# Kernel tuning notes

Measured on AMD Instinct MI355X. Metric: run time of the kernel, lower is better.

The kernel has to match this reference:

```python
import jax, jax.numpy as jnp
import numpy as np

COLOR_SIZE = 8
FILTERS = 64
LAYERS = 4
CUMSUM_NORM = 256 * 256 * 3  # hardcoded in original: /256/256/3


def setup_inputs() -> dict:
    key = jax.random.key(0)
    k0, k1, k2, k3 = jax.random.split(key, 4)
    s = 0.05
    example = jax.random.randint(k0, (4, 256, 256, 3), 0, COLOR_SIZE, dtype=jnp.int32)
    # per-channel Dense stacks: layer 0 has input dim 1, layers 1..3 have input dim FILTERS
    W_in_first = jax.random.normal(k1, (3, 1, FILTERS), dtype=jnp.float32) * s
    b_in_first = jnp.zeros((3, FILTERS), dtype=jnp.float32)
    W_in_rest = jax.random.normal(k2, (LAYERS - 1, 3, FILTERS, FILTERS), dtype=jnp.float32) * s
    b_in_rest = jnp.zeros((LAYERS - 1, 3, FILTERS), dtype=jnp.float32)
    W_final = jax.random.normal(k3, (3, FILTERS, COLOR_SIZE), dtype=jnp.float32) * s
    b_final = jnp.zeros((3, COLOR_SIZE), dtype=jnp.float32)
    return {
        "example": example,
        "W_in_first": W_in_first, "b_in_first": b_in_first,
        "W_in_rest": W_in_rest, "b_in_rest": b_in_rest,
        "W_final": W_final, "b_final": b_final,
    }


def reference(example, W_in_first, b_in_first, W_in_rest, b_in_rest, W_final, b_final):
    # example: [B, H, W, 3] int in [0, COLOR_SIZE)
    x = example.astype(jnp.float32) / COLOR_SIZE * 2.0 - 1.0
    B, H, W, _ = x.shape
    L = H * W
    x = x.reshape(B, L, 3, 1)

    def layer(x, Wl, bl):
        # per-channel dense + relu: [B, L, 3, din] x [3, din, dout] -> [B, L, 3, dout]
        x = jax.nn.relu(jnp.einsum('blcd,cde->blce', x, Wl) + bl)
        # flatten channels into the sequence and take causal running sum
        x = x.reshape(B, L * 3, FILTERS)
        x = jnp.cumsum(x, axis=-2) / CUMSUM_NORM
        return x.reshape(B, L, 3, FILTERS)

    x = layer(x, W_in_first, b_in_first)
    for i in range(LAYERS - 1):
        x = layer(x, W_in_rest[i], b_in_rest[i])

    # final per-channel dense to color logits (no activation)
    x = jnp.einsum('blcd,cde->blce', x, W_final) + b_final
    return x.reshape(B, H, W, 3, COLOR_SIZE)
```

## Files before the change

### kernel.cpp

```cpp
#include <hip/hip_runtime.h>
#include <stdint.h>


#define BB   4
#define SP   65536
#define SS   196608
#define CC   1024
#define NBLK (BB * CC)
#define INVN (1.0f / 196608.0f)

typedef __attribute__((ext_vector_type(8))) _Float16 half8;
typedef __attribute__((ext_vector_type(4))) float    f32x4;

__global__ __launch_bounds__(256)
void prep(const float* __restrict__ W0, const float* __restrict__ b0,
          const float* __restrict__ Wr, const float* __restrict__ Wfin,
          float* __restrict__ Wt32, _Float16* __restrict__ Wt16,
          float* __restrict__ Wf, float* __restrict__ tab)
{
    int i = blockIdx.x * 256 + threadIdx.x;
    int nth = gridDim.x * 256;
    for (int idx = i; idx < 36864; idx += nth) {
        int d = idx & 63, f = (idx >> 6) & 63, lc = idx >> 12;
        float v = Wr[(size_t)(lc * 64 + d) * 64 + f];
        Wt32[idx] = v;
        Wt16[idx] = (_Float16)v;
    }
    for (int idx = i; idx < 1536; idx += nth) {
        int d = idx & 63, k = (idx >> 6) & 7, c = idx >> 9;
        Wf[idx] = Wfin[(size_t)(c * 64 + d) * 8 + k];
    }
    for (int idx = i; idx < 1536; idx += nth) {
        int f = idx & 63, v = (idx >> 6) & 7, c = idx >> 9;
        float xv = v * 0.25f - 1.0f;
        tab[idx] = fmaxf(W0[c * 64 + f] * xv + b0[c * 64 + f], 0.f);
    }
}

__global__ __launch_bounds__(256)
void l0_kernel(const int* __restrict__ ex, _Float16* __restrict__ Y,
               float* __restrict__ A, const float* __restrict__ tab)
{
    __shared__ float stab[1536];
    __shared__ float seg[3][4][64];
    int tid = threadIdx.x;
    for (int i = tid; i < 1536; i += 256) stab[i] = tab[i];
    __syncthreads();

    int b = blockIdx.x / CC, ci = blockIdx.x % CC;
    int f = tid & 63, g = tid >> 6;
    int pixbase = ci * 64 + g * 16;

    float y[3][16];
#pragma unroll
    for (int p = 0; p < 16; ++p) {
        const int* ep = ex + ((size_t)b * SP + pixbase + p) * 3;
#pragma unroll
        for (int c = 0; c < 3; ++c) y[c][p] = stab[(c * 8 + ep[c]) * 64 + f];
    }
#pragma unroll
    for (int c = 0; c < 3; ++c)
#pragma unroll
        for (int p = 1; p < 16; ++p) y[c][p] += y[c][p - 1];

#pragma unroll
    for (int c = 0; c < 3; ++c) seg[c][g][f] = y[c][15];
    __syncthreads();

    float off[3];
#pragma unroll
    for (int c = 0; c < 3; ++c) {
        float o = 0.f;
        for (int g2 = 0; g2 < g; ++g2) o += seg[c][g2][f];
        off[c] = o;
    }
    if (g == 0) {
        float agg = 0.f;
#pragma unroll
        for (int c = 0; c < 3; ++c)
#pragma unroll
            for (int g2 = 0; g2 < 4; ++g2) agg += seg[c][g2][f];
        A[((size_t)b * CC + ci) * 64 + f] = agg;
    }

#pragma unroll
    for (int p = 0; p < 16; ++p) {
        float S0 = y[0][p] + off[0], S1 = y[1][p] + off[1], S2 = y[2][p] + off[2];
        float P1 = p ? y[1][p - 1] + off[1] : off[1];
        float P2 = p ? y[2][p - 1] + off[2] : off[2];
        float r0 = S0 + P1 + P2, r1 = S0 + S1 + P2, r2 = S0 + S1 + S2;
        size_t pix = (size_t)pixbase + p;
        Y[((size_t)(b * 3 + 0) * SP + pix) * 64 + f] = (_Float16)r0;
        Y[((size_t)(b * 3 + 1) * SP + pix) * 64 + f] = (_Float16)r1;
        Y[((size_t)(b * 3 + 2) * SP + pix) * 64 + f] = (_Float16)r2;
    }
}

__global__ __launch_bounds__(1024)
void scanA(const float* __restrict__ A, float* __restrict__ carry)
{
    __shared__ float seg[16][65];
    int b = blockIdx.x, tid = threadIdx.x;
    int f = tid & 63, g = tid >> 6;
    const float* ap = A + (size_t)b * CC * 64;
    float* cp = carry + (size_t)b * CC * 64;
    int j0 = g * 64;
    float sum = 0.f;
#pragma unroll 8
    for (int j = 0; j < 64; ++j) sum += ap[(size_t)(j0 + j) * 64 + f];
    seg[g][f] = sum;
    __syncthreads();
    float run = 0.f;
    for (int g2 = 0; g2 < g; ++g2) run += seg[g2][f];
    for (int j = 0; j < 64; ++j) {
        float v = ap[(size_t)(j0 + j) * 64 + f];
        cp[(size_t)(j0 + j) * 64 + f] = run;
        run += v;
    }
}

__global__ __launch_bounds__(256, 4)
void mid_mfma(const _Float16* Yin, _Float16* Yout,
              const float* __restrict__ carry, float* __restrict__ A,
              const _Float16* __restrict__ W16,
              const float* __restrict__ W32,
              const float* __restrict__ bias)
{
    __shared__ float seg[3][1040];
    __shared__ float basearr[3][64];
    __shared__ float tot[3][64];
    __shared__ _Float16 bounce[64 * 72];

    int b = blockIdx.x / CC, ci = blockIdx.x % CC;
    int tid = threadIdx.x;
    int w = tid >> 6, l = tid & 63;
    int lm = l & 15, lq = l >> 4;
    int p0 = ci * 64 + w * 16;

    if (tid < 192) {
        int c = tid >> 6, f = tid & 63;
        const float* cr = carry + ((size_t)b * CC + ci) * 64;
        const float* wp = W32 + (size_t)(c * 64 + f) * 64;
        float s0 = 0.f, s1 = 0.f, s2 = 0.f, s3 = 0.f;
#pragma unroll
        for (int d4 = 0; d4 < 16; ++d4) {
            float4 cv = *(const float4*)(cr + d4 * 4);
            float4 wv = *(const float4*)(wp + d4 * 4);
            s0 += cv.x * wv.x; s1 += cv.y * wv.y;
            s2 += cv.z * wv.z; s3 += cv.w * wv.w;
        }
        basearr[c][f] = bias[c * 64 + f] + INVN * ((s0 + s1) + (s2 + s3));
    }

    f32x4 acc[3][4];
#pragma unroll
    for (int c = 0; c < 3; ++c) {
        const _Float16* Yc = Yin + ((size_t)(b * 3 + c) * SP) * 64;
        const half8* ap = (const half8*)(Yc + (size_t)(p0 + lm) * 64);
        half8 a0 = ap[lq], a1 = ap[4 + lq];
#pragma unroll
        for (int nt = 0; nt < 4; ++nt) {
            const half8* bp = (const half8*)(W16 + (size_t)(c * 64 + nt * 16 + lm) * 64);
            half8 b0 = bp[lq], b1 = bp[4 + lq];
            f32x4 t = {0.f, 0.f, 0.f, 0.f};
            t = __builtin_amdgcn_mfma_f32_16x16x32_f16(a0, b0, t, 0, 0, 0);
            t = __builtin_amdgcn_mfma_f32_16x16x32_f16(a1, b1, t, 0, 0, 0);
            acc[c][nt] = t;
        }
    }
    __syncthreads();

    float s[3][4][4];
#pragma unroll
    for (int c = 0; c < 3; ++c) {
#pragma unroll
        for (int nt = 0; nt < 4; ++nt) {
            float base = basearr[c][nt * 16 + lm];
            float run = 0.f;
#pragma unroll
            for (int r = 0; r < 4; ++r) {
                float yv = fmaxf(base + INVN * acc[c][nt][r], 0.f);
                run += yv;
                s[c][nt][r] = run;
            }
            seg[c][(w * 4 + lq) * 65 + nt * 16 + lm] = run;
        }
    }
    __syncthreads();

    if (tid < 192) {
        int c = tid >> 6, f = tid & 63;
        float run = 0.f;
#pragma unroll
        for (int sg = 0; sg < 16; ++sg) {
            float v = seg[c][sg * 65 + f];
            seg[c][sg * 65 + f] = run;
            run += v;
        }
        tot[c][f] = run;
    }
    __syncthreads();
    if (tid < 64)
        A[((size_t)b * CC + ci) * 64 + tid] = tot[0][tid] + tot[1][tid] + tot[2][tid];

    float off[3][4];
#pragma unroll
    for (int c = 0; c < 3; ++c)
#pragma unroll
        for (int nt = 0; nt < 4; ++nt)
            off[c][nt] = seg[c][(w * 4 + lq) * 65 + nt * 16 + lm];

#pragma unroll
    for (int cs = 0; cs < 3; ++cs) {
#pragma unroll
        for (int nt = 0; nt < 4; ++nt) {
#pragma unroll
            for (int r = 0; r < 4; ++r) {
                float S0 = off[0][nt] + s[0][nt][r];
                float S1 = off[1][nt] + s[1][nt][r];
                float S2 = off[2][nt] + s[2][nt][r];
                float P1 = off[1][nt] + (r ? s[1][nt][r - 1] : 0.f);
                float P2 = off[2][nt] + (r ? s[2][nt][r - 1] : 0.f);
                float val = (cs == 0) ? S0 + P1 + P2
                          : (cs == 1) ? S0 + S1 + P2
                                      : S0 + S1 + S2;
                bounce[(w * 16 + lq * 4 + r) * 72 + nt * 16 + lm] = (_Float16)val;
            }
        }
        __syncthreads();
        _Float16* Yo = Yout + ((size_t)(b * 3 + cs) * SP + (size_t)ci * 64) * 64;
#pragma unroll
        for (int it = 0; it < 2; ++it) {
            int i8 = it * 256 + tid;
            int pix = i8 >> 3, f8 = i8 & 7;
            *((half8*)Yo + pix * 8 + f8) = *(const half8*)&bounce[pix * 72 + f8 * 8];
        }
        __syncthreads();
    }
}

__global__ __launch_bounds__(192)
void final_kernel(const _Float16* __restrict__ Yin,
                  const float* __restrict__ carry,
                  const float* __restrict__ Wf,
                  const float* __restrict__ bf,
                  float* __restrict__ out)
{
    __shared__ __align__(16) float swf[1536];
    __shared__ float scarry[64];
    __shared__ float pcd[24][8];
    __shared__ float scd[24];
    __shared__ float sbf[24];
    int b = blockIdx.x / CC, ci = blockIdx.x % CC;
    int tid = threadIdx.x;

    for (int i = tid; i < 1536; i += 192) swf[i] = Wf[i];
    if (tid < 64) scarry[tid] = carry[((size_t)b * CC + ci) * 64 + tid];
    if (tid < 24) sbf[tid] = bf[tid];
    __syncthreads();

    {
        int pair = tid >> 3, dg = tid & 7;
        float sx = 0.f;
#pragma unroll
        for (int dd = 0; dd < 8; ++dd) {
            int d = dg * 8 + dd;
            sx += scarry[d] * swf[pair * 64 + d];
        }
        pcd[pair][dg] = sx;
    }
    __syncthreads();
    if (tid < 24) {
        float t = 0.f;
#pragma unroll
        for (int j = 0; j < 8; ++j) t += pcd[tid][j];
        scd[tid] = t;
    }
    __syncthreads();

    int c = tid >> 6, j = tid & 63;
    const half8* xp = (const half8*)(Yin + ((size_t)(b * 3 + c) * SP + ci * 64 + j) * 64);
    half8 h[8];
#pragma unroll
    for (int i = 0; i < 8; ++i) h[i] = xp[i];
    float sk[8];
#pragma unroll
    for (int k = 0; k < 8; ++k) sk[k] = 0.f;
#pragma unroll
    for (int d4 = 0; d4 < 16; ++d4) {
        half8 hv = h[d4 >> 1];
        int o = (d4 & 1) * 4;
        float x0 = (float)hv[o], x1 = (float)hv[o + 1];
        float x2 = (float)hv[o + 2], x3 = (float)hv[o + 3];
#pragma unroll
        for (int k = 0; k < 8; ++k) {
            float4 wv = *(const float4*)&swf[(c * 8 + k) * 64 + d4 * 4];
            sk[k] += x0 * wv.x + x1 * wv.y + x2 * wv.z + x3 * wv.w;
        }
    }
    size_t pos = (size_t)b * SS + (size_t)(ci * 64 + j) * 3 + c;
    float* op = out + pos * 8;
    float o0[8];
#pragma unroll
    for (int k = 0; k < 8; ++k)
        o0[k] = sbf[c * 8 + k] + INVN * (scd[c * 8 + k] + sk[k]);
    *(float4*)(op + 0) = make_float4(o0[0], o0[1], o0[2], o0[3]);
    *(float4*)(op + 4) = make_float4(o0[4], o0[5], o0[6], o0[7]);
}

extern "C" void kernel_launch(void* const* d_in, const int* in_sizes, int n_in,
                              void* d_out, int out_size, void* d_ws, size_t ws_size,
                              hipStream_t stream)
{
    const int*   ex   = (const int*)d_in[0];
    const float* W0   = (const float*)d_in[1];
    const float* b0   = (const float*)d_in[2];
    const float* Wr   = (const float*)d_in[3];
    const float* br   = (const float*)d_in[4];
    const float* Wfin = (const float*)d_in[5];
    const float* bfin = (const float*)d_in[6];
    float* out = (float*)d_out;

    char* ws = (char*)d_ws;
    _Float16* Y = (_Float16*)ws;
    size_t off = (size_t)BB * 3 * SP * 64 * sizeof(_Float16);
    float* A     = (float*)(ws + off);  off += (size_t)BB * CC * 64 * 4;
    float* carry = (float*)(ws + off);  off += (size_t)BB * CC * 64 * 4;
    float* Wt32  = (float*)(ws + off);  off += 36864 * 4;
    float* Wf    = (float*)(ws + off);  off += 1536 * 4;
    float* tab   = (float*)(ws + off);  off += 1536 * 4;
    _Float16* Wt16 = (_Float16*)(ws + off); off += 36864 * 2;

    prep<<<64, 256, 0, stream>>>(W0, b0, Wr, Wfin, Wt32, Wt16, Wf, tab);
    l0_kernel<<<NBLK, 256, 0, stream>>>(ex, Y, A, tab);
    scanA<<<BB, 1024, 0, stream>>>(A, carry);
    for (int l = 0; l < 3; ++l) {
        mid_mfma<<<NBLK, 256, 0, stream>>>(Y, Y, carry, A,
                                           Wt16 + (size_t)l * 12288,
                                           Wt32 + (size_t)l * 12288,
                                           br + (size_t)l * 192);
        scanA<<<BB, 1024, 0, stream>>>(A, carry);
    }
    final_kernel<<<NBLK, 192, 0, stream>>>(Y, carry, Wf, bfin, out);
}
```

Baseline: 414.6 us.

## Process four chunks per block in mid layer with shuffle-based intra-block scan

The mid-layer kernel now handles four 64-pixel chunks per block, cutting the grid by four. Per-thread weight rows are loaded once into registers and reused for the four carry dot products. The LDS-based segment scan is replaced by wave shuffles plus a small per-wave totals table, and all three channel outputs are staged in one larger bounce buffer so they are written with fewer barriers. scanA also gets explicit batched loads for more memory-level parallelism. In exchange the kernel has fewer blocks to spread across the GPU, uses more LDS and registers, and runs its four chunks one after another inside each block.

```diff
diff --git a/kernel.cpp b/kernel.cpp
--- a/kernel.cpp
+++ b/kernel.cpp
@@ -6,7 +6,6 @@
 #define SP   65536
 #define SS   196608
 #define CC   1024
-#define NBLK (BB * CC)
 #define INVN (1.0f / 196608.0f)
 
 typedef __attribute__((ext_vector_type(8))) _Float16 half8;
@@ -106,114 +105,140 @@
     float* cp = carry + (size_t)b * CC * 64;
     int j0 = g * 64;
     float sum = 0.f;
-#pragma unroll 8
-    for (int j = 0; j < 64; ++j) sum += ap[(size_t)(j0 + j) * 64 + f];
+#pragma unroll
+    for (int j8 = 0; j8 < 8; ++j8) {
+        float v[8];
+#pragma unroll
+        for (int k = 0; k < 8; ++k) v[k] = ap[(size_t)(j0 + j8 * 8 + k) * 64 + f];
+#pragma unroll
+        for (int k = 0; k < 8; ++k) sum += v[k];
+    }
     seg[g][f] = sum;
     __syncthreads();
     float run = 0.f;
     for (int g2 = 0; g2 < g; ++g2) run += seg[g2][f];
-    for (int j = 0; j < 64; ++j) {
-        float v = ap[(size_t)(j0 + j) * 64 + f];
-        cp[(size_t)(j0 + j) * 64 + f] = run;
-        run += v;
+#pragma unroll
+    for (int j8 = 0; j8 < 8; ++j8) {
+        float v[8];
+#pragma unroll
+        for (int k = 0; k < 8; ++k) v[k] = ap[(size_t)(j0 + j8 * 8 + k) * 64 + f];
+#pragma unroll
+        for (int k = 0; k < 8; ++k) {
+            cp[(size_t)(j0 + j8 * 8 + k) * 64 + f] = run;
+            run += v[k];
+        }
     }
 }
 
 __global__ __launch_bounds__(256, 4)
-void mid_mfma(const _Float16* Yin, _Float16* Yout,
-              const float* __restrict__ carry, float* __restrict__ A,
-              const _Float16* __restrict__ W16,
-              const float* __restrict__ W32,
-              const float* __restrict__ bias)
-{
-    __shared__ float seg[3][1040];
-    __shared__ float basearr[3][64];
-    __shared__ float tot[3][64];
-    __shared__ _Float16 bounce[64 * 72];
-
-    int b = blockIdx.x / CC, ci = blockIdx.x % CC;
+void mid4(const _Float16* Yin, _Float16* Yout,
+          const float* __restrict__ carry, float* __restrict__ A,
+          const _Float16* __restrict__ W16,
+          const float* __restrict__ W32,
+          const float* __restrict__ bias)
+{
+    __shared__ float basearr4[4][192];
+    __shared__ float wtop[3][4][64];
+    __shared__ __align__(16) _Float16 bounce3[3][64 * 72];
+
     int tid = threadIdx.x;
-    int w = tid >> 6, l = tid & 63;
-    int lm = l & 15, lq = l >> 4;
-    int p0 = ci * 64 + w * 16;
+    int b = blockIdx.x >> 8, cg = blockIdx.x & 255;
+    int w = tid >> 6, ln = tid & 63, lm = ln & 15, lq = ln >> 4;
+    int ci0 = cg * 4;
 
     if (tid < 192) {
         int c = tid >> 6, f = tid & 63;
-        const float* cr = carry + ((size_t)b * CC + ci) * 64;
         const float* wp = W32 + (size_t)(c * 64 + f) * 64;
-        float s0 = 0.f, s1 = 0.f, s2 = 0.f, s3 = 0.f;
-#pragma unroll
-        for (int d4 = 0; d4 < 16; ++d4) {
-            float4 cv = *(const float4*)(cr + d4 * 4);
-            float4 wv = *(const float4*)(wp + d4 * 4);
-            s0 += cv.x * wv.x; s1 += cv.y * wv.y;
-            s2 += cv.z * wv.z; s3 += cv.w * wv.w;
-        }
-        basearr[c][f] = bias[c * 64 + f] + INVN * ((s0 + s1) + (s2 + s3));
-    }
-
-    f32x4 acc[3][4];
-#pragma unroll
-    for (int c = 0; c < 3; ++c) {
-        const _Float16* Yc = Yin + ((size_t)(b * 3 + c) * SP) * 64;
-        const half8* ap = (const half8*)(Yc + (size_t)(p0 + lm) * 64);
-        half8 a0 = ap[lq], a1 = ap[4 + lq];
-#pragma unroll
-        for (int nt = 0; nt < 4; ++nt) {
-            const half8* bp = (const half8*)(W16 + (size_t)(c * 64 + nt * 16 + lm) * 64);
-            half8 b0 = bp[lq], b1 = bp[4 + lq];
-            f32x4 t = {0.f, 0.f, 0.f, 0.f};
-            t = __builtin_amdgcn_mfma_f32_16x16x32_f16(a0, b0, t, 0, 0, 0);
-            t = __builtin_amdgcn_mfma_f32_16x16x32_f16(a1, b1, t, 0, 0, 0);
-            acc[c][nt] = t;
-        }
-    }
-    __syncthreads();
-
-    float s[3][4][4];
-#pragma unroll
-    for (int c = 0; c < 3; ++c) {
-#pragma unroll
-        for (int nt = 0; nt < 4; ++nt) {
-            float base = basearr[c][nt * 16 + lm];
-            float run = 0.f;
-#pragma unroll
-            for (int r = 0; r < 4; ++r) {
-                float yv = fmaxf(base + INVN * acc[c][nt][r], 0.f);
-                run += yv;
-                s[c][nt][r] = run;
-            }
-            seg[c][(w * 4 + lq) * 65 + nt * 16 + lm] = run;
-        }
-    }
-    __syncthreads();
-
-    if (tid < 192) {
-        int c = tid >> 6, f = tid & 63;
-        float run = 0.f;
-#pragma unroll
-        for (int sg = 0; sg < 16; ++sg) {
-            float v = seg[c][sg * 65 + f];
-            seg[c][sg * 65 + f] = run;
-            run += v;
-        }
-        tot[c][f] = run;
-    }
-    __syncthreads();
-    if (tid < 64)
-        A[((size_t)b * CC + ci) * 64 + tid] = tot[0][tid] + tot[1][tid] + tot[2][tid];
-
-    float off[3][4];
-#pragma unroll
-    for (int c = 0; c < 3; ++c)
+        float4 wr[16];
+#pragma unroll
+        for (int d4 = 0; d4 < 16; ++d4) wr[d4] = *(const float4*)(wp + d4 * 4);
+        float bz = bias[c * 64 + f];
+#pragma unroll
+        for (int it = 0; it < 4; ++it) {
+            const float* cr = carry + ((size_t)b * CC + ci0 + it) * 64;
+            float s0 = 0.f, s1 = 0.f, s2 = 0.f, s3 = 0.f;
+#pragma unroll
+            for (int d4 = 0; d4 < 16; ++d4) {
+                float4 cv = *(const float4*)(cr + d4 * 4);
+                s0 += cv.x * wr[d4].x; s1 += cv.y * wr[d4].y;
+                s2 += cv.z * wr[d4].z; s3 += cv.w * wr[d4].w;
+            }
+            basearr4[it][tid] = bz + INVN * ((s0 + s1) + (s2 + s3));
+        }
+    }
+
+    for (int it = 0; it < 4; ++it) {
+        int ci = ci0 + it;
+        int pb = cg * 256 + it * 64;
+        int p0 = pb + w * 16;
+
+        half8 af0[3], af1[3];
+#pragma unroll
+        for (int c = 0; c < 3; ++c) {
+            const half8* ap = (const half8*)(Yin + ((size_t)(b * 3 + c) * SP + p0 + lm) * 64);
+            af0[c] = ap[lq];
+            af1[c] = ap[4 + lq];
+        }
+        f32x4 acc[3][4];
+#pragma unroll
+        for (int c = 0; c < 3; ++c)
+#pragma unroll
+            for (int nt = 0; nt < 4; ++nt) {
+                const half8* bp = (const half8*)(W16 + (size_t)(c * 64 + nt * 16 + lm) * 64);
+                f32x4 t = {0.f, 0.f, 0.f, 0.f};
+                t = __builtin_amdgcn_mfma_f32_16x16x32_f16(af0[c], bp[lq],     t, 0, 0, 0);
+                t = __builtin_amdgcn_mfma_f32_16x16x32_f16(af1[c], bp[4 + lq], t, 0, 0, 0);
+                acc[c][nt] = t;
+            }
+
+        __syncthreads();
+
+        float s[3][4][4], wexcl[3][4];
+#pragma unroll
+        for (int c = 0; c < 3; ++c)
+#pragma unroll
+            for (int nt = 0; nt < 4; ++nt) {
+                float base = basearr4[it][c * 64 + nt * 16 + lm];
+                float run = 0.f;
+#pragma unroll
+                for (int r = 0; r < 4; ++r) {
+                    float yv = fmaxf(base + INVN * acc[c][nt][r], 0.f);
+                    run += yv;
+                    s[c][nt][r] = run;
+                }
+                float v = run;
+                float t1 = __shfl_up(v, 16);
+                if (lq >= 1) v += t1;
+                float t2 = __shfl_up(v, 32);
+                if (lq >= 2) v += t2;
+                wexcl[c][nt] = v - run;
+                if (lq == 3) wtop[c][w][nt * 16 + lm] = v;
+            }
+
+        __syncthreads();
+
+        if (tid < 64) {
+            float agg = 0.f;
+#pragma unroll
+            for (int c = 0; c < 3; ++c)
+#pragma unroll
+                for (int w2 = 0; w2 < 4; ++w2) agg += wtop[c][w2][tid];
+            A[((size_t)b * CC + ci) * 64 + tid] = agg;
+        }
+
+        float off[3][4];
+#pragma unroll
+        for (int c = 0; c < 3; ++c)
+#pragma unroll
+            for (int nt = 0; nt < 4; ++nt) {
+                float o = wexcl[c][nt];
+#pragma unroll
+                for (int w2 = 0; w2 < 3; ++w2)
+                    if (w2 < w) o += wtop[c][w2][nt * 16 + lm];
+                off[c][nt] = o;
+            }
 #pragma unroll
         for (int nt = 0; nt < 4; ++nt)
-            off[c][nt] = seg[c][(w * 4 + lq) * 65 + nt * 16 + lm];
-
-#pragma unroll
-    for (int cs = 0; cs < 3; ++cs) {
-#pragma unroll
-        for (int nt = 0; nt < 4; ++nt) {
 #pragma unroll
             for (int r = 0; r < 4; ++r) {
                 float S0 = off[0][nt] + s[0][nt][r];
@@ -221,21 +246,22 @@
                 float S2 = off[2][nt] + s[2][nt][r];
                 float P1 = off[1][nt] + (r ? s[1][nt][r - 1] : 0.f);
                 float P2 = off[2][nt] + (r ? s[2][nt][r - 1] : 0.f);
-                float val = (cs == 0) ? S0 + P1 + P2
-                          : (cs == 1) ? S0 + S1 + P2
-                                      : S0 + S1 + S2;
-                bounce[(w * 16 + lq * 4 + r) * 72 + nt * 16 + lm] = (_Float16)val;
-            }
-        }
+                int row = w * 16 + lq * 4 + r;
+                bounce3[0][row * 72 + nt * 16 + lm] = (_Float16)(S0 + P1 + P2);
+                bounce3[1][row * 72 + nt * 16 + lm] = (_Float16)(S0 + S1 + P2);
+                bounce3[2][row * 72 + nt * 16 + lm] = (_Float16)(S0 + S1 + S2);
+            }
+
         __syncthreads();
-        _Float16* Yo = Yout + ((size_t)(b * 3 + cs) * SP + (size_t)ci * 64) * 64;
-#pragma unroll
-        for (int it = 0; it < 2; ++it) {
-            int i8 = it * 256 + tid;
-            int pix = i8 >> 3, f8 = i8 & 7;
-            *((half8*)Yo + pix * 8 + f8) = *(const half8*)&bounce[pix * 72 + f8 * 8];
-        }
-        __syncthreads();
+
+#pragma unroll
+        for (int q = 0; q < 6; ++q) {
+            int idx = q * 256 + tid;
+            int c = idx >> 9, rem = idx & 511;
+            int pix = rem >> 3, f8 = rem & 7;
+            half8 v = *(const half8*)&bounce3[c][pix * 72 + f8 * 8];
+            ((half8*)(Yout + ((size_t)(b * 3 + c) * SP + pb + pix) * 64))[f8] = v;
+        }
     }
 }
 
@@ -332,14 +358,14 @@
     _Float16* Wt16 = (_Float16*)(ws + off); off += 36864 * 2;
 
     prep<<<64, 256, 0, stream>>>(W0, b0, Wr, Wfin, Wt32, Wt16, Wf, tab);
-    l0_kernel<<<NBLK, 256, 0, stream>>>(ex, Y, A, tab);
+    l0_kernel<<<BB * CC, 256, 0, stream>>>(ex, Y, A, tab);
     scanA<<<BB, 1024, 0, stream>>>(A, carry);
     for (int l = 0; l < 3; ++l) {
-        mid_mfma<<<NBLK, 256, 0, stream>>>(Y, Y, carry, A,
+        mid4<<<BB * 256, 256, 0, stream>>>(Y, Y, carry, A,
                                            Wt16 + (size_t)l * 12288,
                                            Wt32 + (size_t)l * 12288,
                                            br + (size_t)l * 192);
         scanA<<<BB, 1024, 0, stream>>>(A, carry);
     }
-    final_kernel<<<NBLK, 192, 0, stream>>>(Y, carry, Wf, bfin, out);
-}
+    final_kernel<<<BB * CC, 192, 0, stream>>>(Y, carry, Wf, bfin, out);
+}
```

Result: slower. 577.0 us (+39.2%).
